# Performance work log

Measured on AMD Instinct MI355X. Metric: run time of the kernel, lower is better.

The kernel has to match this reference:

```python
import jax, jax.numpy as jnp
import numpy as np

NUM_GROUPS, GROUP_SIZE, D_MODEL = 8, 4096, 1024
NUM_EXPERTS = 64
EXPERT_CAPACITY = 1024  # capacity_factor 2: 2 * total_tokens / num_experts


def setup_inputs() -> dict:
    key = jax.random.key(0)
    k1, k2, k3 = jax.random.split(key, 3)
    x = jax.random.normal(k1, (NUM_GROUPS, GROUP_SIZE, D_MODEL), dtype=jnp.float32)
    gate_kernel = jax.random.normal(k2, (D_MODEL, NUM_EXPERTS), dtype=jnp.float32) * 0.1
    gate_bias = jax.random.normal(k3, (NUM_EXPERTS,), dtype=jnp.float32) * 0.01
    temperature = jnp.ones((1,), dtype=jnp.float32)
    return {
        "x": x,
        "gate_kernel": gate_kernel,
        "gate_bias": gate_bias,
        "temperature": temperature,
        "expert_capacity": EXPERT_CAPACITY,
    }


def reference(x, gate_kernel, gate_bias, temperature, expert_capacity):
    # x: [G, S, D]; gate_kernel: [D, E]
    G, S, _ = x.shape
    E = gate_kernel.shape[1]

    router_logits = jnp.einsum("gsd,de->gse", x, gate_kernel) + gate_bias  # [G, S, E]
    safe_temp = jnp.maximum(temperature, 0.1)  # [1]
    router_probs = jax.nn.softmax(router_logits / safe_temp, axis=-1)  # [G, S, E]

    # Per-expert top-k over all flattened tokens.
    flat_probs = router_probs.transpose(2, 0, 1).reshape(E, G * S)  # [E, G*S]
    scores, token_indices = jax.lax.top_k(flat_probs, k=expert_capacity)  # [E, C]

    group_indices = token_indices // S  # [E, C]
    pos_indices = token_indices % S  # [E, C]
    expert_ids = jnp.broadcast_to(jnp.arange(E)[:, None], scores.shape)  # [E, C]

    # use_mask_routing=True path: scatter into capacity-limited dense masks.
    expert_masks = jnp.zeros((E, G, S), dtype=jnp.bool_).at[
        expert_ids, group_indices, pos_indices].set(True)
    weight_masks = jnp.zeros((E, G, S), dtype=x.dtype).at[
        expert_ids, group_indices, pos_indices].set(scores)

    loss = jnp.asarray(0.0, dtype=x.dtype)  # training=False
    return expert_masks, weight_masks, loss
```

## Files before the change

kernel.cpp:

```cpp
#include <hip/hip_runtime.h>
#include <math.h>

#define NG 8
#define SEQ 4096
#define DM 1024
#define NE 64
#define GS (NG * SEQ)
#define KSEL 1024
#define MASK_ELEMS (NE * GS)
#define SEG 16
#define SEGLEN (GS / SEG)
#define CAP 2048
#define CAP2 16384

typedef __attribute__((ext_vector_type(8))) short short8;
typedef __attribute__((ext_vector_type(4))) float f32x4;

__device__ __forceinline__ unsigned short f2bf(float v) {
  unsigned u = __float_as_uint(v);
  return (unsigned short)((u + 0x7FFFu + ((u >> 16) & 1u)) >> 16);
}
__device__ __forceinline__ float bf2f(unsigned short h) {
  return __uint_as_float(((unsigned)h) << 16);
}

__global__ __launch_bounds__(256)
void k_split(const float* __restrict__ w, unsigned short* __restrict__ wph,
             unsigned short* __restrict__ wpm, unsigned* __restrict__ zbase) {
  const int t = blockIdx.x * 256 + threadIdx.x;
  if (t < NE * 256 + NE) zbase[t] = 0u;
  const int k = t >> 6, e = t & 63;
  float v = w[t];
  unsigned short h = f2bf(v); float r = v - bf2f(h);
  const int tile = k >> 5, g = (k >> 3) & 3, j = k & 7;
  const int cb = e >> 4, lrow = e & 15;
  const size_t o = (size_t)(tile * 4 + cb) * 512 + (g * 16 + lrow) * 8 + j;
  wph[o] = h; wpm[o] = f2bf(r);
}

__global__ __launch_bounds__(256, 6)
void k_gemm_softmax(const float* __restrict__ x,
                    const unsigned short* __restrict__ wph,
                    const unsigned short* __restrict__ wpm,
                    const float* __restrict__ bias, const float* __restrict__ temp,
                    float* __restrict__ probsT) {
  __shared__ float Lt[4][16][68];
  float (*Pt)[20] = (float (*)[20])&Lt[0][0][0];

  const int tid = threadIdx.x;
  const int w = tid >> 6, lane = tid & 63;
  const int lrow = lane & 15;
  const int g = lane >> 4;
  const int m0 = blockIdx.x * 16;
  const int t0 = w * 8;

  int irow[4], jcol[4];
  {
    union { unsigned short u[8]; short8 v; } ar, on;
#pragma unroll
    for (int j = 0; j < 8; ++j) { ar.u[j] = f2bf((float)lrow); on.u[j] = 0x3F80u; }
    f32x4 z = {0.f, 0.f, 0.f, 0.f};
    f32x4 p1 = __builtin_amdgcn_mfma_f32_16x16x32_bf16(ar.v, on.v, z, 0, 0, 0);
    f32x4 p2 = __builtin_amdgcn_mfma_f32_16x16x32_bf16(on.v, ar.v, z, 0, 0, 0);
#pragma unroll
    for (int b = 0; b < 4; ++b) {
      irow[b] = ((int)p1[b]) >> 5;
      jcol[b] = ((int)p2[b]) >> 5;
    }
  }

  f32x4 acc[4];
#pragma unroll
  for (int cb = 0; cb < 4; ++cb) acc[cb] = (f32x4){0.f, 0.f, 0.f, 0.f};

  const float* aptr = x + (size_t)(m0 + lrow) * DM + g * 8;
  const int boff = lane * 8;

  for (int t = t0; t < t0 + 8; ++t) {
    short8 bh[4], bm[4];
#pragma unroll
    for (int cb = 0; cb < 4; ++cb) {
      const size_t bo = (size_t)(t * 4 + cb) * 512 + boff;
      bh[cb] = *(const short8*)(wph + bo);
      bm[cb] = *(const short8*)(wpm + bo);
    }
    f32x4 a0 = *(const f32x4*)(aptr + t * 32);
    f32x4 a1 = *(const f32x4*)(aptr + t * 32 + 4);
    union { unsigned short u[8]; short8 v; } ah, am;
#pragma unroll
    for (int j = 0; j < 8; ++j) {
      float v0 = (j < 4) ? a0[j] : a1[j - 4];
      unsigned short h_ = f2bf(v0);
      ah.u[j] = h_; am.u[j] = f2bf(v0 - bf2f(h_));
    }
    __builtin_amdgcn_s_setprio(1);
#pragma unroll
    for (int cb = 0; cb < 4; ++cb) {
      acc[cb] = __builtin_amdgcn_mfma_f32_16x16x32_bf16(ah.v, bh[cb], acc[cb], 0, 0, 0);
      acc[cb] = __builtin_amdgcn_mfma_f32_16x16x32_bf16(am.v, bh[cb], acc[cb], 0, 0, 0);
      acc[cb] = __builtin_amdgcn_mfma_f32_16x16x32_bf16(ah.v, bm[cb], acc[cb], 0, 0, 0);
    }
    __builtin_amdgcn_s_setprio(0);
  }

#pragma unroll
  for (int cb = 0; cb < 4; ++cb)
#pragma unroll
    for (int b = 0; b < 4; ++b)
      Lt[w][irow[b]][cb * 16 + jcol[b]] = acc[cb][b];
  __syncthreads();

  float pr[4];
  int tk, q;
  {
    float st = temp[0];
    if (st < 0.1f) st = 0.1f;
    const float inv_t = 1.0f / st;
    tk = tid >> 4; q = tid & 15;
    float l[4];
    float mx = -1.0e30f;
#pragma unroll
    for (int j = 0; j < 4; ++j) {
      const int e = q * 4 + j;
      l[j] = (Lt[0][tk][e] + Lt[1][tk][e] + Lt[2][tk][e] + Lt[3][tk][e] + bias[e]) *
             inv_t;
      mx = fmaxf(mx, l[j]);
    }
    mx = fmaxf(mx, __shfl_xor(mx, 1));
    mx = fmaxf(mx, __shfl_xor(mx, 2));
    mx = fmaxf(mx, __shfl_xor(mx, 4));
    mx = fmaxf(mx, __shfl_xor(mx, 8));
    float p[4], s = 0.0f;
#pragma unroll
    for (int j = 0; j < 4; ++j) { p[j] = __expf(l[j] - mx); s += p[j]; }
    s += __shfl_xor(s, 1);
    s += __shfl_xor(s, 2);
    s += __shfl_xor(s, 4);
    s += __shfl_xor(s, 8);
    const float invs = 1.0f / s;
#pragma unroll
    for (int j = 0; j < 4; ++j) pr[j] = p[j] * invs;
  }
  __syncthreads();
#pragma unroll
  for (int j = 0; j < 4; ++j) Pt[q * 4 + j][tk] = pr[j];
  __syncthreads();

  {
    const int e = tid >> 2, qq = tid & 3;
    *(float4*)(probsT + (size_t)e * GS + m0 + qq * 4) =
        *(const float4*)(&Pt[e][qq * 4]);
  }
}

__device__ __forceinline__ void pick_scan(const unsigned* __restrict__ bins,
                                          unsigned r_in, unsigned& bucket,
                                          unsigned& r_out, unsigned* res) {
  __syncthreads();
  const int tid = threadIdx.x;
  if (tid < 64) {
    uint4 b = ((const uint4*)bins)[tid];
    unsigned s3 = b.w, s2 = b.z + s3, s1 = b.y + s2, s0 = b.x + s1;
    unsigned suf = s0;
#pragma unroll
    for (int off = 1; off < 64; off <<= 1) {
      unsigned t = __shfl_down(suf, off);
      if (tid + off < 64) suf += t;
    }
    unsigned above = suf - s0;
    unsigned inc0 = above + s0, inc1 = above + s1, inc2 = above + s2, inc3 = above + s3;
    if (inc3 >= r_in && inc3 - b.w < r_in) { res[0] = 4 * tid + 3; res[1] = r_in - (inc3 - b.w); }
    if (inc2 >= r_in && inc2 - b.z < r_in) { res[0] = 4 * tid + 2; res[1] = r_in - (inc2 - b.z); }
    if (inc1 >= r_in && inc1 - b.y < r_in) { res[0] = 4 * tid + 1; res[1] = r_in - (inc1 - b.y); }
    if (inc0 >= r_in && inc0 - b.x < r_in) { res[0] = 4 * tid + 0; res[1] = r_in - (inc0 - b.x); }
  }
  __syncthreads();
  bucket = res[0];
  r_out = res[1];
}

__global__ __launch_bounds__(256)
void k_hist0(const float* __restrict__ probsT, unsigned* __restrict__ ghist0) {
  __shared__ unsigned h[4][256];
  const int tid = threadIdx.x, wv = tid >> 6;
  const int e = blockIdx.x >> 4;
  const int seg = blockIdx.x & (SEG - 1);
  h[0][tid] = 0; h[1][tid] = 0; h[2][tid] = 0; h[3][tid] = 0;
  __syncthreads();
  const float4* col = (const float4*)(probsT + (size_t)e * GS + seg * SEGLEN);
#pragma unroll
  for (int i = 0; i < SEGLEN / 1024; ++i) {
    float4 v = col[i * 256 + tid];
    atomicAdd(&h[wv][__float_as_uint(v.x) >> 24], 1u);
    atomicAdd(&h[wv][__float_as_uint(v.y) >> 24], 1u);
    atomicAdd(&h[wv][__float_as_uint(v.z) >> 24], 1u);
    atomicAdd(&h[wv][__float_as_uint(v.w) >> 24], 1u);
  }
  __syncthreads();
  unsigned c = h[0][tid] + h[1][tid] + h[2][tid] + h[3][tid];
  if (c) atomicAdd(&ghist0[e * 256 + tid], c);
}

__global__ __launch_bounds__(256)
void k_compact(const float* __restrict__ probsT, const unsigned* __restrict__ ghist0,
               unsigned* __restrict__ cCnt, int* __restrict__ cIdx,
               float* __restrict__ cKey) {
  __shared__ unsigned res[2];
  __shared__ unsigned locN, basePos;
  __shared__ int locIdx[2048];
  __shared__ float locKey[2048];
  const int tid = threadIdx.x;
  const int e = blockIdx.x >> 4;
  const int seg = blockIdx.x & (SEG - 1);

  if (tid == 0) locN = 0u;
  unsigned b0, r0;
  pick_scan(ghist0 + e * 256, KSEL, b0, r0, res);
  const unsigned blo = (b0 == 0u) ? 0u : (b0 - 1u);

  const float* col = probsT + (size_t)e * GS + seg * SEGLEN;
  for (int i = 0; i < SEGLEN / 256; ++i) {
    const int t = i * 256 + tid;
    const float p = col[t];
    if ((__float_as_uint(p) >> 24) >= blo) {
      unsigned pos = atomicAdd(&locN, 1u);
      locIdx[pos] = seg * SEGLEN + t;
      locKey[pos] = p;
    }
  }
  __syncthreads();
  if (tid == 0) basePos = locN ? atomicAdd(&cCnt[e], locN) : 0u;
  __syncthreads();
  const unsigned n = locN, bp = basePos;
  for (unsigned i = tid; i < n; i += 256) {
    const unsigned gp = bp + i;
    if (gp < CAP2) {
      cIdx[(size_t)e * CAP2 + gp] = locIdx[i];
      cKey[(size_t)e * CAP2 + gp] = locKey[i];
    }
  }
}

__global__ __launch_bounds__(256)
void k_select2(const unsigned* __restrict__ ghist0, const unsigned* __restrict__ cCnt,
               const int* __restrict__ cIdx, const float* __restrict__ cKey,
               const float* __restrict__ temp, unsigned* __restrict__ defCnt,
               unsigned* __restrict__ candCnt, int* __restrict__ candIdx,
               float* __restrict__ thrHiA) {
  __shared__ unsigned res[2];
  __shared__ unsigned h[4][256];
  __shared__ unsigned hs[256];
  __shared__ unsigned nd, nc;
  const int tid = threadIdx.x, wv = tid >> 6;
  const int e = blockIdx.x;
  const int cnt = (int)min(cCnt[e], (unsigned)CAP2);

  unsigned b0, r;
  pick_scan(ghist0 + e * 256, KSEL, b0, r, res);
  unsigned pfx = b0 << 24;

  for (int pass = 1; pass < 4; ++pass) {
    const int shift = 24 - 8 * pass;
    const unsigned hm = 0xFFFFFFFFu << (shift + 8);
    for (int i = tid; i < 1024; i += 256) ((unsigned*)h)[i] = 0u;
    __syncthreads();
    for (int i = tid; i < cnt; i += 256) {
      unsigned key = __float_as_uint(cKey[(size_t)e * CAP2 + i]);
      if ((key & hm) == (pfx & hm)) atomicAdd(&h[wv][(key >> shift) & 255], 1u);
    }
    __syncthreads();
    hs[tid] = h[0][tid] + h[1][tid] + h[2][tid] + h[3][tid];
    unsigned b, rn;
    pick_scan(hs, r, b, rn, res);
    pfx |= b << shift;
    r = rn;
  }

  const float thrv = __uint_as_float(pfx);
  float st = temp[0];
  if (st < 0.1f) st = 0.1f;
  const float rel = 2.0e-3f / st;
  const float hi = thrv * (1.0f + rel);
  const float lo = thrv * (1.0f - rel);
  if (tid == 0) thrHiA[e] = hi;

  if (tid == 0) { nd = 0u; nc = 0u; }
  __syncthreads();
  for (int i = tid; i < cnt; i += 256) {
    const float p = cKey[(size_t)e * CAP2 + i];
    const int t = cIdx[(size_t)e * CAP2 + i];
    if (p > hi) {
      atomicAdd(&nd, 1u);
    } else if (p >= lo) {
      unsigned pos = atomicAdd(&nc, 1u);
      if (pos < CAP) candIdx[e * CAP + pos] = t;
    }
  }
  __syncthreads();
  if (tid == 0) {
    defCnt[e] = nd;
    candCnt[e] = min(nc, (unsigned)CAP);
  }
}

__global__ __launch_bounds__(256)
void k_repair(const float* __restrict__ x, const float* __restrict__ w,
              const float* __restrict__ bias, const float* __restrict__ temp,
              const unsigned* __restrict__ candCnt, const int* __restrict__ candIdx,
              double* __restrict__ candKey) {
  __shared__ double red[4][64];
  const int e = blockIdx.x >> 4;
  const int chunk = blockIdx.x & 15;
  const int tid = threadIdx.x;
  const int ee = tid & 63, q = tid >> 6;
  const int cnt = (int)min(candCnt[e], (unsigned)CAP);

  double st = (double)temp[0];
  if (st < 0.1) st = 0.1;
  const double inv_t = 1.0 / st;

  for (int i = chunk; i < cnt; i += 16) {
    const int t = candIdx[e * CAP + i];
    const float* xr = x + (size_t)t * DM;
    double s0 = 0.0, s1 = 0.0, s2 = 0.0, s3 = 0.0;
    const int kb = q * 256;
    for (int k = kb; k < kb + 256; k += 4) {
      s0 += (double)xr[k + 0] * (double)w[(size_t)(k + 0) * NE + ee];
      s1 += (double)xr[k + 1] * (double)w[(size_t)(k + 1) * NE + ee];
      s2 += (double)xr[k + 2] * (double)w[(size_t)(k + 2) * NE + ee];
      s3 += (double)xr[k + 3] * (double)w[(size_t)(k + 3) * NE + ee];
    }
    red[q][ee] = (s0 + s1) + (s2 + s3);
    __syncthreads();
    if (tid < 64) {
      double l = (red[0][tid] + red[1][tid] + red[2][tid] + red[3][tid] +
                  (double)bias[tid]) * inv_t;
      double m = l;
#pragma unroll
      for (int off = 1; off < 64; off <<= 1) m = fmax(m, __shfl_xor(m, off));
      double ex = exp(l - m);
      double ss = ex;
#pragma unroll
      for (int off = 1; off < 64; off <<= 1) ss += __shfl_xor(ss, off);
      if (tid == e) candKey[e * CAP + i] = ex / ss;
    }
    __syncthreads();
  }
}

__global__ __launch_bounds__(256)
void k_scatter(const float* __restrict__ probsT, const float* __restrict__ thrHiA,
               float* __restrict__ out) {
  const int gid = blockIdx.x * 256 + threadIdx.x;
  const int base = gid * 4;
  const int e = base >> 15;
  float4 p = *(const float4*)(probsT + (size_t)base);
  const float hi = thrHiA[e];
  float pv[4] = {p.x, p.y, p.z, p.w};
  float mk[4], wt[4];
#pragma unroll
  for (int c = 0; c < 4; ++c) {
    bool sel = pv[c] > hi;
    mk[c] = sel ? 1.0f : 0.0f;
    wt[c] = sel ? pv[c] : 0.0f;
  }
  *(float4*)(out + (size_t)base) = make_float4(mk[0], mk[1], mk[2], mk[3]);
  *(float4*)(out + (size_t)MASK_ELEMS + base) = make_float4(wt[0], wt[1], wt[2], wt[3]);
  if (gid == 0) out[2 * (size_t)MASK_ELEMS] = 0.0f;
}

__global__ __launch_bounds__(256)
void k_finish(const unsigned* __restrict__ defCnt, const unsigned* __restrict__ candCnt,
              const int* __restrict__ candIdx, const double* __restrict__ candKey,
              const float* __restrict__ probsT, float* __restrict__ out) {
  __shared__ double kd[CAP];
  __shared__ int ti[CAP];
  const int e = blockIdx.x, tid = threadIdx.x;
  const int cnt = (int)min(candCnt[e], (unsigned)CAP);
  const int need = KSEL - (int)defCnt[e];

  for (int i = tid; i < cnt; i += 256) {
    kd[i] = candKey[e * CAP + i];
    ti[i] = candIdx[e * CAP + i];
  }
  __syncthreads();
  for (int i = tid; i < cnt; i += 256) {
    const double ki = kd[i];
    const int tii = ti[i];
    int rank = 0;
    for (int j = 0; j < cnt; ++j)
      rank += (kd[j] > ki) || (kd[j] == ki && ti[j] < tii);
    if (rank < need) {
      out[(size_t)e * GS + tii] = 1.0f;
      out[(size_t)MASK_ELEMS + (size_t)e * GS + tii] = probsT[(size_t)e * GS + tii];
    }
  }
}

extern "C" void kernel_launch(void* const* d_in, const int* in_sizes, int n_in,
                              void* d_out, int out_size, void* d_ws, size_t ws_size,
                              hipStream_t stream) {
  const float* x    = (const float*)d_in[0];
  const float* gw   = (const float*)d_in[1];
  const float* gb   = (const float*)d_in[2];
  const float* temp = (const float*)d_in[3];

  float* probsT    = (float*)d_ws;
  unsigned* ghist0 = (unsigned*)((char*)d_ws + (size_t)MASK_ELEMS * 4);
  unsigned* cCnt   = ghist0 + NE * 256;
  unsigned* defCnt = cCnt + NE;
  unsigned* candCnt = defCnt + NE;
  float* thrHiA    = (float*)(candCnt + NE);
  int* candIdx     = (int*)(thrHiA + NE);
  double* candKey  = (double*)(candIdx + NE * CAP);
  int* cIdx        = (int*)(candKey + NE * CAP);
  float* cKey      = (float*)(cIdx + (size_t)NE * CAP2);
  unsigned short* wph = (unsigned short*)(cKey + (size_t)NE * CAP2);
  unsigned short* wpm = wph + DM * NE;

  k_split<<<DM * NE / 256, 256, 0, stream>>>(gw, wph, wpm, ghist0);
  k_gemm_softmax<<<GS / 16, 256, 0, stream>>>(x, wph, wpm, gb, temp, probsT);
  k_hist0<<<NE * SEG, 256, 0, stream>>>(probsT, ghist0);
  k_compact<<<NE * SEG, 256, 0, stream>>>(probsT, ghist0, cCnt, cIdx, cKey);
  k_select2<<<NE, 256, 0, stream>>>(ghist0, cCnt, cIdx, cKey, temp, defCnt,
                                    candCnt, candIdx, thrHiA);
  k_repair<<<NE * 16, 256, 0, stream>>>(x, gw, gb, temp, candCnt, candIdx, candKey);
  k_scatter<<<MASK_ELEMS / 1024, 256, 0, stream>>>(probsT, thrHiA, (float*)d_out);
  k_finish<<<NE, 256, 0, stream>>>(defCnt, candCnt, candIdx, candKey,
                                   probsT, (float*)d_out);
}
```

Before: 105.6 us.

## Stage gate weights in double-buffered LDS and process 32 tokens per block

The router GEMM block now covers 32 tokens instead of 16. Its four waves are split into two token groups times two K halves, and the bf16 hi/lo weight tiles are staged through a double-buffered 32KB shared-memory buffer with register prefetch. Each block previously re-read the whole weight matrix from global memory; the new layout shares each weight load across two token tiles and overlaps the global loads with MFMA work. The softmax reduction is reworked to combine two partial-K accumulators with 8 experts per thread. In exchange there are per-iteration barriers, more LDS use, and a lower occupancy bound (launch bounds 3).

```diff
diff --git a/kernel.cpp b/kernel.cpp
--- a/kernel.cpp
+++ b/kernel.cpp
@@ -38,21 +38,21 @@
   wph[o] = h; wpm[o] = f2bf(r);
 }
 
-__global__ __launch_bounds__(256, 6)
+__global__ __launch_bounds__(256, 3)
 void k_gemm_softmax(const float* __restrict__ x,
                     const unsigned short* __restrict__ wph,
                     const unsigned short* __restrict__ wpm,
                     const float* __restrict__ bias, const float* __restrict__ temp,
                     float* __restrict__ probsT) {
+  __shared__ __align__(16) unsigned char Bs[2][16384];
   __shared__ float Lt[4][16][68];
-  float (*Pt)[20] = (float (*)[20])&Lt[0][0][0];
+  float (*Pt)[36] = (float (*)[36])&Bs[0][0];
 
   const int tid = threadIdx.x;
   const int w = tid >> 6, lane = tid & 63;
-  const int lrow = lane & 15;
-  const int g = lane >> 4;
-  const int m0 = blockIdx.x * 16;
-  const int t0 = w * 8;
+  const int tg = w >> 1, kh = w & 1;
+  const int lrow = lane & 15, g = lane >> 4;
+  const int m0 = blockIdx.x * 32 + tg * 16;
 
   int irow[4], jcol[4];
   {
@@ -73,35 +73,73 @@
 #pragma unroll
   for (int cb = 0; cb < 4; ++cb) acc[cb] = (f32x4){0.f, 0.f, 0.f, 0.f};
 
+  const char* wpb0 = (const char*)wph;
+  const char* wpb1 = (const char*)wpm;
+  uint4 sreg[4];
+
+#define LOADS(i)                                                                     \
+  {                                                                                  \
+    _Pragma("unroll")                                                                \
+    for (int q = 0; q < 4; ++q) {                                                    \
+      const char* src = (q & 1) ? wpb1 : wpb0;                                       \
+      sreg[q] = *(const uint4*)(src + (((size_t)(q >> 1) * 16 + (i)) << 12) +        \
+                                tid * 16);                                           \
+    }                                                                                \
+  }
+
+#define WRITES(bi)                                                                   \
+  {                                                                                  \
+    _Pragma("unroll")                                                                \
+    for (int q = 0; q < 4; ++q)                                                      \
+      *(uint4*)(&Bs[bi][q * 4096 + tid * 16]) = sreg[q];                             \
+  }
+
   const float* aptr = x + (size_t)(m0 + lrow) * DM + g * 8;
-  const int boff = lane * 8;
-
-  for (int t = t0; t < t0 + 8; ++t) {
-    short8 bh[4], bm[4];
-#pragma unroll
-    for (int cb = 0; cb < 4; ++cb) {
-      const size_t bo = (size_t)(t * 4 + cb) * 512 + boff;
-      bh[cb] = *(const short8*)(wph + bo);
-      bm[cb] = *(const short8*)(wpm + bo);
-    }
-    f32x4 a0 = *(const f32x4*)(aptr + t * 32);
-    f32x4 a1 = *(const f32x4*)(aptr + t * 32 + 4);
-    union { unsigned short u[8]; short8 v; } ah, am;
+  f32x4 aA[2][2];
+
+#define LOADA(i, pa)                                                                 \
+  {                                                                                  \
+    const f32x4* ap = (const f32x4*)(aptr + (kh * 16 + (i)) * 32);                   \
+    aA[pa][0] = ap[0]; aA[pa][1] = ap[1];                                            \
+  }
+
+  LOADS(0);
+  WRITES(0);
+  LOADS(1);
+  LOADA(0, 0);
+  LOADA(1, 1);
+
+  union { unsigned short u[8]; short8 v; } ah, am;
+#pragma unroll
+  for (int i = 0; i < 16; ++i) {
+    __syncthreads();
 #pragma unroll
     for (int j = 0; j < 8; ++j) {
-      float v0 = (j < 4) ? a0[j] : a1[j - 4];
+      float v0 = (j < 4) ? aA[i & 1][0][j] : aA[i & 1][1][j - 4];
       unsigned short h_ = f2bf(v0);
       ah.u[j] = h_; am.u[j] = f2bf(v0 - bf2f(h_));
     }
-    __builtin_amdgcn_s_setprio(1);
-#pragma unroll
-    for (int cb = 0; cb < 4; ++cb) {
-      acc[cb] = __builtin_amdgcn_mfma_f32_16x16x32_bf16(ah.v, bh[cb], acc[cb], 0, 0, 0);
-      acc[cb] = __builtin_amdgcn_mfma_f32_16x16x32_bf16(am.v, bh[cb], acc[cb], 0, 0, 0);
-      acc[cb] = __builtin_amdgcn_mfma_f32_16x16x32_bf16(ah.v, bm[cb], acc[cb], 0, 0, 0);
-    }
-    __builtin_amdgcn_s_setprio(0);
-  }
+    if (i + 1 < 16) WRITES((i & 1) ^ 1);
+    if (i + 2 < 16) {
+      LOADS(i + 2);
+      LOADA(i + 2, i & 1);
+    }
+    {
+      const unsigned char* bb = &Bs[i & 1][kh * 8192];
+#pragma unroll
+      for (int cb = 0; cb < 4; ++cb) {
+        short8 bh_ = *(const short8*)(bb + cb * 1024 + lane * 16);
+        short8 bm_ = *(const short8*)(bb + 4096 + cb * 1024 + lane * 16);
+        acc[cb] = __builtin_amdgcn_mfma_f32_16x16x32_bf16(ah.v, bh_, acc[cb], 0, 0, 0);
+        acc[cb] = __builtin_amdgcn_mfma_f32_16x16x32_bf16(am.v, bh_, acc[cb], 0, 0, 0);
+        acc[cb] = __builtin_amdgcn_mfma_f32_16x16x32_bf16(ah.v, bm_, acc[cb], 0, 0, 0);
+      }
+    }
+  }
+
+#undef LOADS
+#undef WRITES
+#undef LOADA
 
 #pragma unroll
   for (int cb = 0; cb < 4; ++cb)
@@ -110,46 +148,40 @@
       Lt[w][irow[b]][cb * 16 + jcol[b]] = acc[cb][b];
   __syncthreads();
 
-  float pr[4];
-  int tk, q;
   {
     float st = temp[0];
     if (st < 0.1f) st = 0.1f;
     const float inv_t = 1.0f / st;
-    tk = tid >> 4; q = tid & 15;
-    float l[4];
+    const int tb = tid >> 3, q8 = tid & 7;
+    const int tgt = tb >> 4, t16 = tb & 15;
+    float l[8];
     float mx = -1.0e30f;
 #pragma unroll
-    for (int j = 0; j < 4; ++j) {
-      const int e = q * 4 + j;
-      l[j] = (Lt[0][tk][e] + Lt[1][tk][e] + Lt[2][tk][e] + Lt[3][tk][e] + bias[e]) *
-             inv_t;
+    for (int j = 0; j < 8; ++j) {
+      const int e = q8 * 8 + j;
+      l[j] = (Lt[tgt * 2][t16][e] + Lt[tgt * 2 + 1][t16][e] + bias[e]) * inv_t;
       mx = fmaxf(mx, l[j]);
     }
     mx = fmaxf(mx, __shfl_xor(mx, 1));
     mx = fmaxf(mx, __shfl_xor(mx, 2));
     mx = fmaxf(mx, __shfl_xor(mx, 4));
-    mx = fmaxf(mx, __shfl_xor(mx, 8));
-    float p[4], s = 0.0f;
-#pragma unroll
-    for (int j = 0; j < 4; ++j) { p[j] = __expf(l[j] - mx); s += p[j]; }
+    float p[8], s = 0.0f;
+#pragma unroll
+    for (int j = 0; j < 8; ++j) { p[j] = __expf(l[j] - mx); s += p[j]; }
     s += __shfl_xor(s, 1);
     s += __shfl_xor(s, 2);
     s += __shfl_xor(s, 4);
-    s += __shfl_xor(s, 8);
     const float invs = 1.0f / s;
 #pragma unroll
-    for (int j = 0; j < 4; ++j) pr[j] = p[j] * invs;
-  }
-  __syncthreads();
-#pragma unroll
-  for (int j = 0; j < 4; ++j) Pt[q * 4 + j][tk] = pr[j];
+    for (int j = 0; j < 8; ++j) Pt[q8 * 8 + j][tb] = p[j] * invs;
+  }
   __syncthreads();
 
   {
     const int e = tid >> 2, qq = tid & 3;
-    *(float4*)(probsT + (size_t)e * GS + m0 + qq * 4) =
-        *(const float4*)(&Pt[e][qq * 4]);
+    float* dst = probsT + (size_t)e * GS + blockIdx.x * 32 + qq * 8;
+    *(float4*)dst = *(const float4*)(&Pt[e][qq * 8]);
+    *(float4*)(dst + 4) = *(const float4*)(&Pt[e][qq * 8 + 4]);
   }
 }
 
@@ -419,7 +451,7 @@
   unsigned short* wpm = wph + DM * NE;
 
   k_split<<<DM * NE / 256, 256, 0, stream>>>(gw, wph, wpm, ghist0);
-  k_gemm_softmax<<<GS / 16, 256, 0, stream>>>(x, wph, wpm, gb, temp, probsT);
+  k_gemm_softmax<<<GS / 32, 256, 0, stream>>>(x, wph, wpm, gb, temp, probsT);
   k_hist0<<<NE * SEG, 256, 0, stream>>>(probsT, ghist0);
   k_compact<<<NE * SEG, 256, 0, stream>>>(probsT, ghist0, cCnt, cIdx, cKey);
   k_select2<<<NE, 256, 0, stream>>>(ghist0, cCnt, cIdx, cKey, temp, defCnt,
```

Measured after the change: 146.2 us. 38.5% more time.

## Tile router GEMM over 64 rows per block with double-buffered loads

Applied to the files above, without the earlier changes.

Each block of the gate GEMM+softmax kernel now handles 64 tokens instead of 16. Every wave keeps a 4x4 grid of MFMA accumulators, so each loaded weight fragment is reused across four row fragments. Global loads for the next K step are issued before the MFMAs of the current step in a two-stage software pipeline. This cuts redundant weight loads and hides load latency, at the cost of much higher register and LDS use, lower occupancy (launch bounds 2), and 4x fewer blocks (512).

```diff
diff --git a/kernel.cpp b/kernel.cpp
--- a/kernel.cpp
+++ b/kernel.cpp
@@ -38,21 +38,19 @@
   wph[o] = h; wpm[o] = f2bf(r);
 }
 
-__global__ __launch_bounds__(256, 6)
+__global__ __launch_bounds__(256, 2)
 void k_gemm_softmax(const float* __restrict__ x,
                     const unsigned short* __restrict__ wph,
                     const unsigned short* __restrict__ wpm,
                     const float* __restrict__ bias, const float* __restrict__ temp,
                     float* __restrict__ probsT) {
-  __shared__ float Lt[4][16][68];
-  float (*Pt)[20] = (float (*)[20])&Lt[0][0][0];
+  __shared__ float Lt[4][64][68];
+  float (*Pt)[68] = (float (*)[68])&Lt[0][0][0];
 
   const int tid = threadIdx.x;
   const int w = tid >> 6, lane = tid & 63;
-  const int lrow = lane & 15;
-  const int g = lane >> 4;
-  const int m0 = blockIdx.x * 16;
-  const int t0 = w * 8;
+  const int lrow = lane & 15, g = lane >> 4;
+  const int m0 = blockIdx.x * 64;
 
   int irow[4], jcol[4];
   {
@@ -69,87 +67,125 @@
     }
   }
 
-  f32x4 acc[4];
-#pragma unroll
-  for (int cb = 0; cb < 4; ++cb) acc[cb] = (f32x4){0.f, 0.f, 0.f, 0.f};
-
-  const float* aptr = x + (size_t)(m0 + lrow) * DM + g * 8;
+  f32x4 acc[4][4];
+#pragma unroll
+  for (int rf = 0; rf < 4; ++rf)
+#pragma unroll
+    for (int cb = 0; cb < 4; ++cb) acc[rf][cb] = (f32x4){0.f, 0.f, 0.f, 0.f};
+
   const int boff = lane * 8;
-
-  for (int t = t0; t < t0 + 8; ++t) {
-    short8 bh[4], bm[4];
-#pragma unroll
-    for (int cb = 0; cb < 4; ++cb) {
-      const size_t bo = (size_t)(t * 4 + cb) * 512 + boff;
-      bh[cb] = *(const short8*)(wph + bo);
-      bm[cb] = *(const short8*)(wpm + bo);
-    }
-    f32x4 a0 = *(const f32x4*)(aptr + t * 32);
-    f32x4 a1 = *(const f32x4*)(aptr + t * 32 + 4);
-    union { unsigned short u[8]; short8 v; } ah, am;
-#pragma unroll
-    for (int j = 0; j < 8; ++j) {
-      float v0 = (j < 4) ? a0[j] : a1[j - 4];
-      unsigned short h_ = f2bf(v0);
-      ah.u[j] = h_; am.u[j] = f2bf(v0 - bf2f(h_));
-    }
-    __builtin_amdgcn_s_setprio(1);
-#pragma unroll
-    for (int cb = 0; cb < 4; ++cb) {
-      acc[cb] = __builtin_amdgcn_mfma_f32_16x16x32_bf16(ah.v, bh[cb], acc[cb], 0, 0, 0);
-      acc[cb] = __builtin_amdgcn_mfma_f32_16x16x32_bf16(am.v, bh[cb], acc[cb], 0, 0, 0);
-      acc[cb] = __builtin_amdgcn_mfma_f32_16x16x32_bf16(ah.v, bm[cb], acc[cb], 0, 0, 0);
-    }
-    __builtin_amdgcn_s_setprio(0);
-  }
-
-#pragma unroll
-  for (int cb = 0; cb < 4; ++cb)
-#pragma unroll
-    for (int b = 0; b < 4; ++b)
-      Lt[w][irow[b]][cb * 16 + jcol[b]] = acc[cb][b];
-  __syncthreads();
-
-  float pr[4];
-  int tk, q;
+  const int T0 = w * 8;
+
+  f32x4 aP[4][2], aQ[4][2];
+  short8 bhP[4], bmP[4], bhQ[4], bmQ[4];
+
+#define LOADA_(T, ar)                                                                \
+  {                                                                                  \
+    _Pragma("unroll")                                                                \
+    for (int rf = 0; rf < 4; ++rf) {                                                 \
+      const f32x4* ap = (const f32x4*)(x + (size_t)(m0 + rf * 16 + lrow) * DM +      \
+                                       (T) * 32 + g * 8);                            \
+      ar[rf][0] = ap[0]; ar[rf][1] = ap[1];                                          \
+    }                                                                                \
+  }
+
+#define LOADB_(T, bh, bm)                                                            \
+  {                                                                                  \
+    _Pragma("unroll")                                                                \
+    for (int cb = 0; cb < 4; ++cb) {                                                 \
+      const size_t bo = (size_t)((T) * 4 + cb) * 512 + boff;                         \
+      bh[cb] = *(const short8*)(wph + bo);                                           \
+      bm[cb] = *(const short8*)(wpm + bo);                                           \
+    }                                                                                \
+  }
+
+#define SPLIT_MFMA(ar, bh, bm)                                                       \
+  {                                                                                  \
+    _Pragma("unroll")                                                                \
+    for (int rf = 0; rf < 4; ++rf) {                                                 \
+      union { unsigned short u[8]; short8 v; } ah, am;                               \
+      _Pragma("unroll")                                                              \
+      for (int j = 0; j < 8; ++j) {                                                  \
+        float v0 = (j < 4) ? ar[rf][0][j] : ar[rf][1][j - 4];                        \
+        unsigned short h_ = f2bf(v0);                                                \
+        ah.u[j] = h_; am.u[j] = f2bf(v0 - bf2f(h_));                                 \
+      }                                                                              \
+      _Pragma("unroll")                                                              \
+      for (int cb = 0; cb < 4; ++cb) {                                               \
+        acc[rf][cb] = __builtin_amdgcn_mfma_f32_16x16x32_bf16(ah.v, bh[cb],          \
+                                                              acc[rf][cb], 0, 0, 0); \
+        acc[rf][cb] = __builtin_amdgcn_mfma_f32_16x16x32_bf16(am.v, bh[cb],          \
+                                                              acc[rf][cb], 0, 0, 0); \
+        acc[rf][cb] = __builtin_amdgcn_mfma_f32_16x16x32_bf16(ah.v, bm[cb],          \
+                                                              acc[rf][cb], 0, 0, 0); \
+      }                                                                              \
+    }                                                                                \
+  }
+
+  LOADA_(T0, aP);
+  LOADB_(T0, bhP, bmP);
+#pragma unroll
+  for (int t = 0; t < 8; t += 2) {
+    LOADA_(T0 + t + 1, aQ);
+    LOADB_(T0 + t + 1, bhQ, bmQ);
+    SPLIT_MFMA(aP, bhP, bmP);
+    if (t + 2 < 8) {
+      LOADA_(T0 + t + 2, aP);
+      LOADB_(T0 + t + 2, bhP, bmP);
+    }
+    SPLIT_MFMA(aQ, bhQ, bmQ);
+  }
+
+#undef LOADA_
+#undef LOADB_
+#undef SPLIT_MFMA
+
+#pragma unroll
+  for (int rf = 0; rf < 4; ++rf)
+#pragma unroll
+    for (int cb = 0; cb < 4; ++cb)
+#pragma unroll
+      for (int b = 0; b < 4; ++b)
+        Lt[w][rf * 16 + irow[b]][cb * 16 + jcol[b]] = acc[rf][cb][b];
+  __syncthreads();
+
+  float pr[16];
+  const int tk = tid >> 2, q = tid & 3;
   {
     float st = temp[0];
     if (st < 0.1f) st = 0.1f;
     const float inv_t = 1.0f / st;
-    tk = tid >> 4; q = tid & 15;
-    float l[4];
+    float l[16];
     float mx = -1.0e30f;
 #pragma unroll
-    for (int j = 0; j < 4; ++j) {
-      const int e = q * 4 + j;
+    for (int j = 0; j < 16; ++j) {
+      const int e = q * 16 + j;
       l[j] = (Lt[0][tk][e] + Lt[1][tk][e] + Lt[2][tk][e] + Lt[3][tk][e] + bias[e]) *
              inv_t;
       mx = fmaxf(mx, l[j]);
     }
     mx = fmaxf(mx, __shfl_xor(mx, 1));
     mx = fmaxf(mx, __shfl_xor(mx, 2));
-    mx = fmaxf(mx, __shfl_xor(mx, 4));
-    mx = fmaxf(mx, __shfl_xor(mx, 8));
-    float p[4], s = 0.0f;
-#pragma unroll
-    for (int j = 0; j < 4; ++j) { p[j] = __expf(l[j] - mx); s += p[j]; }
+    float p[16], s = 0.0f;
+#pragma unroll
+    for (int j = 0; j < 16; ++j) { p[j] = __expf(l[j] - mx); s += p[j]; }
     s += __shfl_xor(s, 1);
     s += __shfl_xor(s, 2);
-    s += __shfl_xor(s, 4);
-    s += __shfl_xor(s, 8);
     const float invs = 1.0f / s;
 #pragma unroll
-    for (int j = 0; j < 4; ++j) pr[j] = p[j] * invs;
-  }
-  __syncthreads();
-#pragma unroll
-  for (int j = 0; j < 4; ++j) Pt[q * 4 + j][tk] = pr[j];
+    for (int j = 0; j < 16; ++j) pr[j] = p[j] * invs;
+  }
+  __syncthreads();
+#pragma unroll
+  for (int j = 0; j < 16; ++j) Pt[q * 16 + j][tk] = pr[j];
   __syncthreads();
 
   {
     const int e = tid >> 2, qq = tid & 3;
-    *(float4*)(probsT + (size_t)e * GS + m0 + qq * 4) =
-        *(const float4*)(&Pt[e][qq * 4]);
+    float* dst = probsT + (size_t)e * GS + m0 + qq * 16;
+#pragma unroll
+    for (int c2 = 0; c2 < 4; ++c2)
+      *(float4*)(dst + c2 * 4) = *(const float4*)(&Pt[e][qq * 16 + c2 * 4]);
   }
 }
 
@@ -419,7 +455,7 @@
   unsigned short* wpm = wph + DM * NE;
 
   k_split<<<DM * NE / 256, 256, 0, stream>>>(gw, wph, wpm, ghist0);
-  k_gemm_softmax<<<GS / 16, 256, 0, stream>>>(x, wph, wpm, gb, temp, probsT);
+  k_gemm_softmax<<<GS / 64, 256, 0, stream>>>(x, wph, wpm, gb, temp, probsT);
   k_hist0<<<NE * SEG, 256, 0, stream>>>(probsT, ghist0);
   k_compact<<<NE * SEG, 256, 0, stream>>>(probsT, ghist0, cCnt, cIdx, cKey);
   k_select2<<<NE, 256, 0, stream>>>(ghist0, cCnt, cIdx, cKey, temp, defCnt,
```

New measurement: 95.20 us. 1.11x faster.
